# Performance work log

Measured on AMD Instinct MI355X. Metric: run time of the kernel, lower is better.

## Reference

```python
import jax, jax.numpy as jnp
import numpy as np

MIN_NORM = 1e-15
EPS = 4e-3  # fp32 boundary epsilon used by HGCN PoincareBall


def _norm(x):
    return jnp.maximum(jnp.linalg.norm(x, axis=-1, keepdims=True), MIN_NORM)


def _artanh(x):
    return jnp.arctanh(jnp.clip(x, -1.0 + 1e-7, 1.0 - 1e-7))


def proj(x, c):
    # clip points to the open Poincare ball of curvature c
    norm = _norm(x)
    maxnorm = (1.0 - EPS) / jnp.sqrt(c)
    return jnp.where(norm > maxnorm, x / norm * maxnorm, x)


def expmap0(u, c):
    sc = jnp.sqrt(c)
    un = _norm(u)
    return jnp.tanh(sc * un) * u / (sc * un)


def logmap0(p, c):
    sc = jnp.sqrt(c)
    pn = _norm(p)
    return _artanh(sc * pn) * p / (pn * sc)


def mobius_add(x, y, c):
    x2 = jnp.sum(x * x, axis=-1, keepdims=True)
    y2 = jnp.sum(y * y, axis=-1, keepdims=True)
    xy = jnp.sum(x * y, axis=-1, keepdims=True)
    num = (1.0 + 2.0 * c * xy + c * y2) * x + (1.0 - c * x2) * y
    den = 1.0 + 2.0 * c * xy + (c ** 2) * x2 * y2
    return num / jnp.maximum(den, MIN_NORM)


def _mobius_from_mx(mx, x, c):
    # shared tail of mobius_matvec: mx is the Euclidean product, x the input points
    sc = jnp.sqrt(c)
    x_norm = _norm(x)            # [..., 1]
    mx_norm = _norm(mx)          # [..., 1]
    res = jnp.tanh(mx_norm / x_norm * _artanh(sc * x_norm)) * mx / (mx_norm * sc)
    zero_row = jnp.all(mx == 0, axis=-1, keepdims=True)
    return jnp.where(zero_row, jnp.zeros_like(res), res)


def mobius_matvec(m, x, c):
    # standard form: mx = x @ m^T   (m: [out, in], x: [N, in])
    return _mobius_from_mx(x @ m.T, x, c)


def hyp_linear(x, W, b, c):
    hw = proj(expmap0(W, c), c)             # proj_tan0 is identity on PoincareBall
    res = proj(mobius_matvec(hw, x, c), c)
    hb = proj(expmap0(b[None, :], c), c)
    return proj(mobius_add(res, hb, c), c)


def hyp_agg(h, adj, W, b, c):
    hw = proj(expmap0(W, c), c)
    support = mobius_matvec(hw, h, c)       # [N, O]
    # mobius_matvec(support, adj, c): Euclidean part is adj @ support,
    # hyperbolic rescale uses row norms of adj (the 'x' argument)
    out = _mobius_from_mx(adj @ support, adj, c)
    out = mobius_add(out, b[None, :], c)    # raw Euclidean bias, as in source
    return proj(out, c)


def hyp_act(h, c):
    xt = jax.nn.leaky_relu(logmap0(h, c))   # default slope 0.01 == F.leaky_relu
    return proj(expmap0(xt, c), 1.0 - c)    # NOTE: source projects with 1-c


def setup_inputs() -> dict:
    key = jax.random.key(0)
    kx, ka, kw1, kw2, kb2 = jax.random.split(key, 5)
    N, IN, OUT = 8192, 512, 128
    x = jax.random.normal(kx, (N, IN), dtype=jnp.float32) * 0.1
    adj = jax.random.uniform(ka, (N, N), dtype=jnp.float32) * (1.0 / N)
    c = jnp.full((1,), 0.7, dtype=jnp.float32)
    glorot = np.sqrt(6.0 / (IN + OUT))
    lin_weight = jax.random.uniform(kw1, (OUT, IN), minval=-glorot, maxval=glorot, dtype=jnp.float32)
    lin_bias = jnp.zeros((OUT,), dtype=jnp.float32)
    stdv = 1.0 / np.sqrt(OUT)
    agg_weight = jax.random.uniform(kw2, (OUT, OUT), minval=-stdv, maxval=stdv, dtype=jnp.float32)
    agg_bias = jax.random.uniform(kb2, (OUT,), minval=-stdv, maxval=stdv, dtype=jnp.float32)
    return {"x": x, "adj": adj, "c": c, "lin_weight": lin_weight, "lin_bias": lin_bias,
            "agg_weight": agg_weight, "agg_bias": agg_bias}


def reference(x, adj, c, lin_weight, lin_bias, agg_weight, agg_bias):
    h = hyp_linear(x, lin_weight, lin_bias, c)
    h = hyp_agg(h, adj, agg_weight, agg_bias, c)
    return hyp_act(h, c)
```

## Files before the change

### kernel.cpp

```cpp
#include <hip/hip_runtime.h>
#include <math.h>


#define MINN 1e-15f

typedef __bf16 bf16x8 __attribute__((ext_vector_type(8)));
typedef float  f32x4  __attribute__((ext_vector_type(4)));

__device__ __forceinline__ unsigned short f2bf(float f) {
  unsigned int u = __float_as_uint(f);
  u += 0x7FFFu + ((u >> 16) & 1u);
  return (unsigned short)(u >> 16);
}

__device__ __forceinline__ unsigned pk_trunc(float lo, float hi) {
  return __builtin_amdgcn_perm(__float_as_uint(hi), __float_as_uint(lo),
                               0x07060302u);
}

__device__ __forceinline__ float artanh_clip(float z) {
  const float B = (float)(1.0 - 1e-7);
  z = fminf(fmaxf(z, -B), B);
  return 0.5f * logf((1.0f + z) / (1.0f - z));
}

__device__ __forceinline__ float red16(float v) {
  v += __shfl_xor(v, 1, 16);
  v += __shfl_xor(v, 2, 16);
  v += __shfl_xor(v, 4, 16);
  v += __shfl_xor(v, 8, 16);
  return v;
}
__device__ __forceinline__ int red16_and(int v) {
  v &= __shfl_xor(v, 1, 16);
  v &= __shfl_xor(v, 2, 16);
  v &= __shfl_xor(v, 4, 16);
  v &= __shfl_xor(v, 8, 16);
  return v;
}

__device__ __forceinline__ float block_reduce_128(float v, float* red, int t) {
  #pragma unroll
  for (int m = 1; m < 64; m <<= 1) v += __shfl_xor(v, m, 64);
  if ((t & 63) == 0) red[t >> 6] = v;
  __syncthreads();
  return red[0] + red[1];
}

__device__ __forceinline__ size_t bswz(int k, int n) {
  return ((size_t)(((k >> 5) * 8 + (n >> 4)) * 64 + ((k >> 3) & 3) * 16 +
                   (n & 15))) * 8 + (k & 7);
}

__global__ __launch_bounds__(128) void prep_kernel(
    const float* __restrict__ lw, const float* __restrict__ aw,
    const float* __restrict__ lb, const float* __restrict__ cp,
    unsigned short* __restrict__ B1, unsigned short* __restrict__ B2,
    float* __restrict__ hb)
{
  const float c  = cp[0];
  const float sc = sqrtf(c);
  const float maxn = 0.996f / sc;
  const int b = blockIdx.x, t = threadIdx.x;
  __shared__ float red[2];

  if (b < 128) {
    const int o = b;
    float4 v = ((const float4*)(lw + (size_t)o * 512))[t];
    float ss = block_reduce_128(v.x*v.x + v.y*v.y + v.z*v.z + v.w*v.w, red, t);
    float un = fmaxf(sqrtf(ss), MINN);
    float f  = tanhf(sc * un) / (sc * un);
    float nn = f * un;
    if (nn > maxn) f *= maxn / nn;
    float vals[4] = {v.x, v.y, v.z, v.w};
    #pragma unroll
    for (int i = 0; i < 4; ++i)
      B1[bswz(4 * t + i, o)] = f2bf(f * vals[i]);
  } else if (b < 256) {
    const int n = b - 128;
    float v = aw[(size_t)n * 128 + t];
    float ss = block_reduce_128(v * v, red, t);
    float un = fmaxf(sqrtf(ss), MINN);
    float f  = tanhf(sc * un) / (sc * un);
    float nn = f * un;
    if (nn > maxn) f *= maxn / nn;
    B2[bswz(t, n)] = f2bf(f * v);
  } else {
    float v = lb[t];
    float ss = block_reduce_128(v * v, red, t);
    float un = fmaxf(sqrtf(ss), MINN);
    float f  = tanhf(sc * un) / (sc * un);
    float nn = f * un;
    if (nn > maxn) f *= maxn / nn;
    hb[t] = f * v;
  }
}

__global__ __launch_bounds__(256, 2) void hyp_fused12(
    const float* __restrict__ x, const bf16x8* __restrict__ B1f,
    const bf16x8* __restrict__ B2f, const float* __restrict__ cp,
    const float* __restrict__ hbv, unsigned short* __restrict__ B3)
{
  __shared__ __align__(16) float part[4][16][132];
  __shared__ float asw[4][16];
  __shared__ __align__(16) unsigned short h_lds[16][136];
  const int t = threadIdx.x;
  const int w = t >> 6, lane = t & 63;
  const int quad = lane >> 4, l15 = lane & 15;
  const int row0 = blockIdx.x * 16;
  const float c = cp[0], sc = sqrtf(c), maxn = 0.996f / sc;

  f32x4 acc[8] = {};
  float as4[4] = {};
  const float*  Ap = x + (size_t)(row0 + l15) * 512 + w * 128 + quad * 8;
  const bf16x8* Bp = B1f + (size_t)(w * 4) * 512 + lane;

  #pragma unroll
  for (int s = 0; s < 4; ++s) {
    float4 x0 = *(const float4*)(Ap + s * 32);
    float4 x1 = *(const float4*)(Ap + s * 32 + 4);
    as4[0] = fmaf(x0.x, x0.x, fmaf(x0.y, x0.y, as4[0]));
    as4[1] = fmaf(x0.z, x0.z, fmaf(x0.w, x0.w, as4[1]));
    as4[2] = fmaf(x1.x, x1.x, fmaf(x1.y, x1.y, as4[2]));
    as4[3] = fmaf(x1.z, x1.z, fmaf(x1.w, x1.w, as4[3]));
    union { unsigned short us[8]; bf16x8 v; } pk;
    pk.us[0] = f2bf(x0.x); pk.us[1] = f2bf(x0.y);
    pk.us[2] = f2bf(x0.z); pk.us[3] = f2bf(x0.w);
    pk.us[4] = f2bf(x1.x); pk.us[5] = f2bf(x1.y);
    pk.us[6] = f2bf(x1.z); pk.us[7] = f2bf(x1.w);
    #pragma unroll
    for (int i = 0; i < 8; ++i)
      acc[i] = __builtin_amdgcn_mfma_f32_16x16x32_bf16(
                   pk.v, Bp[(size_t)s * 512 + i * 64], acc[i], 0, 0, 0);
  }
  float asum = (as4[0] + as4[1]) + (as4[2] + as4[3]);
  asum += __shfl_xor(asum, 16, 64);
  asum += __shfl_xor(asum, 32, 64);
  #pragma unroll
  for (int i = 0; i < 8; ++i)
    #pragma unroll
    for (int r = 0; r < 4; ++r)
      part[w][quad * 4 + r][i * 16 + l15] = acc[i][r];
  if (lane < 16) asw[w][l15] = asum;
  __syncthreads();

  const int row = t >> 4, j0 = t & 15;
  float v[8];
  #pragma unroll
  for (int i = 0; i < 8; ++i)
    v[i] = part[0][row][j0 * 8 + i] + part[1][row][j0 * 8 + i]
         + part[2][row][j0 * 8 + i] + part[3][row][j0 * 8 + i];
  const float xss = asw[0][row] + asw[1][row] + asw[2][row] + asw[3][row];

  float mxss_l = 0.f; int zf = 1;
  #pragma unroll
  for (int i = 0; i < 8; ++i) { mxss_l += v[i] * v[i]; zf &= (v[i] == 0.f); }
  const float mxss = red16(mxss_l);
  zf = red16_and(zf);

  const float xn  = fmaxf(sqrtf(xss), MINN);
  const float mxn = fmaxf(sqrtf(mxss), MINN);
  float f1 = 0.f;
  if (!zf) f1 = tanhf(mxn / xn * artanh_clip(sc * xn)) / (mxn * sc);

  float g = f1;
  {
    float rn = f1 * mxn;
    if (rn > maxn) g = f1 * (maxn / rn);
  }
  float yv[8];
  {
    float4 q0 = ((const float4*)hbv)[j0 * 2];
    float4 q1 = ((const float4*)hbv)[j0 * 2 + 1];
    yv[0]=q0.x; yv[1]=q0.y; yv[2]=q0.z; yv[3]=q0.w;
    yv[4]=q1.x; yv[5]=q1.y; yv[6]=q1.z; yv[7]=q1.w;
  }
  float xy_l = 0.f, y2_l = 0.f, o8[8];
  #pragma unroll
  for (int i = 0; i < 8; ++i) {
    o8[i] = g * v[i];
    xy_l += o8[i] * yv[i];
    y2_l += yv[i] * yv[i];
  }
  const float xy = red16(xy_l), y2 = red16(y2_l);
  const float x2 = g * g * mxss;
  const float den = fmaxf(1.0f + 2.0f * c * xy + c * c * x2 * y2, MINN);
  const float ca = (1.0f + 2.0f * c * xy + c * y2) / den;
  const float cb = (1.0f - c * x2) / den;
  float h8[8]; float hss_l = 0.f;
  #pragma unroll
  for (int i = 0; i < 8; ++i) {
    h8[i] = ca * o8[i] + cb * yv[i];
    hss_l += h8[i] * h8[i];
  }
  const float hss = red16(hss_l);
  const float hn  = fmaxf(sqrtf(hss), MINN);
  const float s2  = (hn > maxn) ? maxn / hn : 1.0f;
  const float hn2 = fmaxf(s2 * hn, MINN);

  {
    union { unsigned short us[8]; uint4 q; } hp;
    #pragma unroll
    for (int i = 0; i < 8; ++i) hp.us[i] = f2bf(s2 * h8[i]);
    *(uint4*)&h_lds[row][j0 * 8] = hp.q;
  }
  __syncthreads();

  const bf16x8 av2 = *(const bf16x8*)&h_lds[l15][w * 32 + quad * 8];
  f32x4 acc2[8] = {};
  #pragma unroll
  for (int i = 0; i < 8; ++i)
    acc2[i] = __builtin_amdgcn_mfma_f32_16x16x32_bf16(
                  av2, B2f[(size_t)(w * 8 + i) * 64 + lane], acc2[i], 0, 0, 0);
  #pragma unroll
  for (int i = 0; i < 8; ++i)
    #pragma unroll
    for (int r = 0; r < 4; ++r)
      part[w][quad * 4 + r][i * 16 + l15] = acc2[i][r];
  __syncthreads();

  float v2[8];
  #pragma unroll
  for (int i = 0; i < 8; ++i)
    v2[i] = part[0][row][j0 * 8 + i] + part[1][row][j0 * 8 + i]
          + part[2][row][j0 * 8 + i] + part[3][row][j0 * 8 + i];
  float m2l = 0.f; int zf2 = 1;
  #pragma unroll
  for (int i = 0; i < 8; ++i) { m2l += v2[i] * v2[i]; zf2 &= (v2[i] == 0.f); }
  const float mx2ss = red16(m2l);
  zf2 = red16_and(zf2);
  const float mx2n = fmaxf(sqrtf(mx2ss), MINN);
  float f2 = 0.f;
  if (!zf2) f2 = tanhf(mx2n / hn2 * artanh_clip(sc * hn2)) / (mx2n * sc);

  const int k = row0 + row;
  const size_t base = ((size_t)(((k >> 5) * 8 + (j0 >> 1)) * 64 +
                       ((k >> 3) & 3) * 16 + 8 * (j0 & 1))) * 8 + (k & 7);
  #pragma unroll
  for (int i = 0; i < 8; ++i)
    B3[base + (size_t)i * 8] = f2bf(f2 * v2[i]);
}

__global__ __launch_bounds__(512, 2) void hyp_gemm3(
    const float* __restrict__ A, const bf16x8* __restrict__ Bf,
    const float* __restrict__ cp, const float* __restrict__ yvec,
    float* __restrict__ out)
{
  __shared__ __align__(16) unsigned short a_lds[2][32][264];
  const int t = threadIdx.x;
  const int w = t >> 6, lane = t & 63;
  const int quad = lane >> 4, l15 = lane & 15;
  const int wm = w >> 2, wn = w & 3;
  const int row0 = blockIdx.x * 32;
  const float c = cp[0], sc = sqrtf(c), maxn = 0.996f / sc;

  f32x4 acc[2] = {};
  float as4[4] = {};
  const float* Ap = A + (size_t)(row0 + 4 * w) * 8192 + lane * 4;
  const bf16x8* Bw = Bf + (size_t)(2 * wn) * 64 + lane;

  {
    float4 aR[4];
    #pragma unroll
    for (int j = 0; j < 4; ++j) aR[j] = *(const float4*)(Ap + j * 8192);
    #pragma unroll
    for (int j = 0; j < 4; ++j) {
      as4[j] = fmaf(aR[j].x, aR[j].x, fmaf(aR[j].y, aR[j].y,
               fmaf(aR[j].z, aR[j].z, fmaf(aR[j].w, aR[j].w, as4[j]))));
      *(uint2*)&a_lds[0][4 * w + j][lane * 4] =
          make_uint2(pk_trunc(aR[j].x, aR[j].y), pk_trunc(aR[j].z, aR[j].w));
    }
  }
  __syncthreads();

  for (int win = 0; win < 32; ++win) {
    const int cur = win & 1;
    bf16x8 b[8][2];
    #pragma unroll
    for (int ks = 0; ks < 8; ++ks) {
      b[ks][0] = Bw[(size_t)((win * 8 + ks) * 8 + 0) * 64];
      b[ks][1] = Bw[(size_t)((win * 8 + ks) * 8 + 1) * 64];
    }
    float4 aR[4];
    if (win < 31) {
      #pragma unroll
      for (int j = 0; j < 4; ++j)
        aR[j] = *(const float4*)(Ap + j * 8192 + (size_t)(win + 1) * 256);
    }
    #pragma unroll
    for (int ks = 0; ks < 8; ++ks) {
      bf16x8 af = *(const bf16x8*)
          &a_lds[cur][16 * wm + l15][ks * 32 + quad * 8];
      acc[0] = __builtin_amdgcn_mfma_f32_16x16x32_bf16(af, b[ks][0], acc[0],
                                                       0, 0, 0);
      acc[1] = __builtin_amdgcn_mfma_f32_16x16x32_bf16(af, b[ks][1], acc[1],
                                                       0, 0, 0);
    }
    if (win < 31) {
      #pragma unroll
      for (int j = 0; j < 4; ++j) {
        as4[j] = fmaf(aR[j].x, aR[j].x, fmaf(aR[j].y, aR[j].y,
                 fmaf(aR[j].z, aR[j].z, fmaf(aR[j].w, aR[j].w, as4[j]))));
        *(uint2*)&a_lds[cur ^ 1][4 * w + j][lane * 4] =
            make_uint2(pk_trunc(aR[j].x, aR[j].y), pk_trunc(aR[j].z, aR[j].w));
      }
    }
    __syncthreads();
  }

  float (*part)[132] = (float (*)[132]) & a_lds[0][0][0];
  float* asw = (float*)&a_lds[0][0][0] + 32 * 132;

  #pragma unroll
  for (int i = 0; i < 2; ++i)
    #pragma unroll
    for (int r = 0; r < 4; ++r)
      part[16 * wm + quad * 4 + r][32 * wn + 16 * i + l15] = acc[i][r];
  #pragma unroll
  for (int j = 0; j < 4; ++j) {
    float s = as4[j];
    #pragma unroll
    for (int m = 1; m < 64; m <<= 1) s += __shfl_xor(s, m, 64);
    if (lane == 0) asw[4 * w + j] = s;
  }
  __syncthreads();

  const int row = t >> 4, j0 = t & 15;
  float v[8];
  {
    float4 q0 = *(const float4*)&part[row][j0 * 8];
    float4 q1 = *(const float4*)&part[row][j0 * 8 + 4];
    v[0]=q0.x; v[1]=q0.y; v[2]=q0.z; v[3]=q0.w;
    v[4]=q1.x; v[5]=q1.y; v[6]=q1.z; v[7]=q1.w;
  }
  const float xss = asw[row];

  float mxss_l = 0.f; int zf = 1;
  #pragma unroll
  for (int i = 0; i < 8; ++i) { mxss_l += v[i] * v[i]; zf &= (v[i] == 0.f); }
  const float mxss = red16(mxss_l);
  zf = red16_and(zf);

  const float xn  = fmaxf(sqrtf(xss), MINN);
  const float mxn = fmaxf(sqrtf(mxss), MINN);
  float f1 = 0.f;
  if (!zf) f1 = tanhf(mxn / xn * artanh_clip(sc * xn)) / (mxn * sc);

  float yv[8];
  {
    float4 q0 = ((const float4*)yvec)[j0 * 2];
    float4 q1 = ((const float4*)yvec)[j0 * 2 + 1];
    yv[0]=q0.x; yv[1]=q0.y; yv[2]=q0.z; yv[3]=q0.w;
    yv[4]=q1.x; yv[5]=q1.y; yv[6]=q1.z; yv[7]=q1.w;
  }

  float xy_l = 0.f, y2_l = 0.f, o8[8];
  #pragma unroll
  for (int i = 0; i < 8; ++i) {
    o8[i] = f1 * v[i];
    xy_l += o8[i] * yv[i];
    y2_l += yv[i] * yv[i];
  }
  const float xy = red16(xy_l), y2 = red16(y2_l);
  const float x2 = f1 * f1 * mxss;
  const float den = fmaxf(1.0f + 2.0f * c * xy + c * c * x2 * y2, MINN);
  const float ca = (1.0f + 2.0f * c * xy + c * y2) / den;
  const float cb = (1.0f - c * x2) / den;
  float h8[8]; float hss_l = 0.f;
  #pragma unroll
  for (int i = 0; i < 8; ++i) {
    h8[i] = ca * o8[i] + cb * yv[i];
    hss_l += h8[i] * h8[i];
  }
  const float hss = red16(hss_l);
  const float hn  = fmaxf(sqrtf(hss), MINN);
  const float s2  = (hn > maxn) ? maxn / hn : 1.0f;

  const float pn = fmaxf(s2 * hn, MINN);
  const float lf = artanh_clip(sc * pn) / (pn * sc);
  float xt[8]; float uss_l = 0.f;
  #pragma unroll
  for (int i = 0; i < 8; ++i) {
    float l = lf * (s2 * h8[i]);
    xt[i] = (l >= 0.f) ? l : 0.01f * l;
    uss_l += xt[i] * xt[i];
  }
  const float uss = red16(uss_l);
  const float un  = fmaxf(sqrtf(uss), MINN);
  const float ef  = tanhf(sc * un) / (sc * un);
  const float on  = ef * un;
  const float maxn2 = 0.996f / sqrtf(1.0f - c);
  const float s3 = (on > maxn2) ? maxn2 / on : 1.0f;

  float* orow = out + (size_t)(row0 + row) * 128 + j0 * 8;
  *(float4*)orow =
      make_float4(s3*ef*xt[0], s3*ef*xt[1], s3*ef*xt[2], s3*ef*xt[3]);
  *(float4*)(orow + 4) =
      make_float4(s3*ef*xt[4], s3*ef*xt[5], s3*ef*xt[6], s3*ef*xt[7]);
}

extern "C" void kernel_launch(void* const* d_in, const int* in_sizes, int n_in,
                              void* d_out, int out_size, void* d_ws, size_t ws_size,
                              hipStream_t stream)
{
  const float* x   = (const float*)d_in[0];
  const float* adj = (const float*)d_in[1];
  const float* cp  = (const float*)d_in[2];
  const float* lw  = (const float*)d_in[3];
  const float* lb  = (const float*)d_in[4];
  const float* aw  = (const float*)d_in[5];
  const float* ab  = (const float*)d_in[6];
  float* out = (float*)d_out;

  char* ws = (char*)d_ws;
  unsigned short* B1sw = (unsigned short*)(ws);
  unsigned short* B2sw = (unsigned short*)(ws + 131072);
  unsigned short* B3sw = (unsigned short*)(ws + 163840);
  float*          hb   = (float*)(ws + 2260992);

  prep_kernel<<<257, 128, 0, stream>>>(lw, aw, lb, cp, B1sw, B2sw, hb);
  hyp_fused12<<<512, 256, 0, stream>>>(x, (const bf16x8*)B1sw,
                                       (const bf16x8*)B2sw, cp, hb, B3sw);
  hyp_gemm3<<<256, 512, 0, stream>>>(adj, (const bf16x8*)B3sw, cp, ab, out);
}
```

Measured before the change: 408.3 us.

## Halve gemm3 row tile to 16 rows and double grid for more blocks

The adjacency GEMM kernel now handles 16 rows per block instead of 32. Each of its 8 waves computes one 16-column output tile, and the grid doubles to 512 blocks. Launch bounds ask for 4 blocks per CU, aiming to spread the 8192x8192 fp32 adj stream over more CUs and waves so more memory loads are in flight. In exchange every block reads the whole bf16 B3 matrix, so B traffic doubles, and half the threads sit idle in the epilogue.

Result: no change. 407.1 us (-0.3%).

```diff
diff --git a/kernel.cpp b/kernel.cpp
--- a/kernel.cpp
+++ b/kernel.cpp
@@ -241,33 +241,32 @@
     B3[base + (size_t)i * 8] = f2bf(f2 * v2[i]);
 }
 
-__global__ __launch_bounds__(512, 2) void hyp_gemm3(
+__global__ __launch_bounds__(512, 4) void hyp_gemm3(
     const float* __restrict__ A, const bf16x8* __restrict__ Bf,
     const float* __restrict__ cp, const float* __restrict__ yvec,
     float* __restrict__ out)
 {
-  __shared__ __align__(16) unsigned short a_lds[2][32][264];
+  __shared__ __align__(16) unsigned short a_lds[2][16][264];
   const int t = threadIdx.x;
   const int w = t >> 6, lane = t & 63;
   const int quad = lane >> 4, l15 = lane & 15;
-  const int wm = w >> 2, wn = w & 3;
-  const int row0 = blockIdx.x * 32;
+  const int row0 = blockIdx.x * 16;
   const float c = cp[0], sc = sqrtf(c), maxn = 0.996f / sc;
 
-  f32x4 acc[2] = {};
-  float as4[4] = {};
-  const float* Ap = A + (size_t)(row0 + 4 * w) * 8192 + lane * 4;
-  const bf16x8* Bw = Bf + (size_t)(2 * wn) * 64 + lane;
-
-  {
-    float4 aR[4];
-    #pragma unroll
-    for (int j = 0; j < 4; ++j) aR[j] = *(const float4*)(Ap + j * 8192);
-    #pragma unroll
-    for (int j = 0; j < 4; ++j) {
-      as4[j] = fmaf(aR[j].x, aR[j].x, fmaf(aR[j].y, aR[j].y,
-               fmaf(aR[j].z, aR[j].z, fmaf(aR[j].w, aR[j].w, as4[j]))));
-      *(uint2*)&a_lds[0][4 * w + j][lane * 4] =
+  f32x4 acc = {};
+  float as2[2] = {};
+  const float*  Ap = A + (size_t)(row0 + 2 * w) * 8192 + lane * 4;
+  const bf16x8* Bw = Bf + (size_t)w * 64 + lane;
+
+  {
+    float4 aR[2];
+    #pragma unroll
+    for (int j = 0; j < 2; ++j) aR[j] = *(const float4*)(Ap + j * 8192);
+    #pragma unroll
+    for (int j = 0; j < 2; ++j) {
+      as2[j] = fmaf(aR[j].x, aR[j].x, fmaf(aR[j].y, aR[j].y,
+               fmaf(aR[j].z, aR[j].z, fmaf(aR[j].w, aR[j].w, as2[j]))));
+      *(uint2*)&a_lds[0][2 * w + j][lane * 4] =
           make_uint2(pk_trunc(aR[j].x, aR[j].y), pk_trunc(aR[j].z, aR[j].w));
     }
   }
@@ -275,33 +274,27 @@
 
   for (int win = 0; win < 32; ++win) {
     const int cur = win & 1;
-    bf16x8 b[8][2];
-    #pragma unroll
-    for (int ks = 0; ks < 8; ++ks) {
-      b[ks][0] = Bw[(size_t)((win * 8 + ks) * 8 + 0) * 64];
-      b[ks][1] = Bw[(size_t)((win * 8 + ks) * 8 + 1) * 64];
-    }
-    float4 aR[4];
+    bf16x8 b[8];
+    #pragma unroll
+    for (int ks = 0; ks < 8; ++ks)
+      b[ks] = Bw[(size_t)(win * 8 + ks) * 512];
+    float4 aR[2];
     if (win < 31) {
       #pragma unroll
-      for (int j = 0; j < 4; ++j)
+      for (int j = 0; j < 2; ++j)
         aR[j] = *(const float4*)(Ap + j * 8192 + (size_t)(win + 1) * 256);
     }
     #pragma unroll
     for (int ks = 0; ks < 8; ++ks) {
-      bf16x8 af = *(const bf16x8*)
-          &a_lds[cur][16 * wm + l15][ks * 32 + quad * 8];
-      acc[0] = __builtin_amdgcn_mfma_f32_16x16x32_bf16(af, b[ks][0], acc[0],
-                                                       0, 0, 0);
-      acc[1] = __builtin_amdgcn_mfma_f32_16x16x32_bf16(af, b[ks][1], acc[1],
-                                                       0, 0, 0);
+      bf16x8 af = *(const bf16x8*)&a_lds[cur][l15][ks * 32 + quad * 8];
+      acc = __builtin_amdgcn_mfma_f32_16x16x32_bf16(af, b[ks], acc, 0, 0, 0);
     }
     if (win < 31) {
       #pragma unroll
-      for (int j = 0; j < 4; ++j) {
-        as4[j] = fmaf(aR[j].x, aR[j].x, fmaf(aR[j].y, aR[j].y,
-                 fmaf(aR[j].z, aR[j].z, fmaf(aR[j].w, aR[j].w, as4[j]))));
-        *(uint2*)&a_lds[cur ^ 1][4 * w + j][lane * 4] =
+      for (int j = 0; j < 2; ++j) {
+        as2[j] = fmaf(aR[j].x, aR[j].x, fmaf(aR[j].y, aR[j].y,
+                 fmaf(aR[j].z, aR[j].z, fmaf(aR[j].w, aR[j].w, as2[j]))));
+        *(uint2*)&a_lds[cur ^ 1][2 * w + j][lane * 4] =
             make_uint2(pk_trunc(aR[j].x, aR[j].y), pk_trunc(aR[j].z, aR[j].w));
       }
     }
@@ -309,22 +302,21 @@
   }
 
   float (*part)[132] = (float (*)[132]) & a_lds[0][0][0];
-  float* asw = (float*)&a_lds[0][0][0] + 32 * 132;
-
-  #pragma unroll
-  for (int i = 0; i < 2; ++i)
-    #pragma unroll
-    for (int r = 0; r < 4; ++r)
-      part[16 * wm + quad * 4 + r][32 * wn + 16 * i + l15] = acc[i][r];
-  #pragma unroll
-  for (int j = 0; j < 4; ++j) {
-    float s = as4[j];
+  float* asw = (float*)&a_lds[0][0][0] + 16 * 132;
+
+  #pragma unroll
+  for (int r = 0; r < 4; ++r)
+    part[quad * 4 + r][16 * w + l15] = acc[r];
+  #pragma unroll
+  for (int j = 0; j < 2; ++j) {
+    float s = as2[j];
     #pragma unroll
     for (int m = 1; m < 64; m <<= 1) s += __shfl_xor(s, m, 64);
-    if (lane == 0) asw[4 * w + j] = s;
-  }
-  __syncthreads();
-
+    if (lane == 0) asw[2 * w + j] = s;
+  }
+  __syncthreads();
+
+  if (t >= 256) return;
   const int row = t >> 4, j0 = t & 15;
   float v[8];
   {
@@ -421,5 +413,5 @@
   prep_kernel<<<257, 128, 0, stream>>>(lw, aw, lb, cp, B1sw, B2sw, hb);
   hyp_fused12<<<512, 256, 0, stream>>>(x, (const bf16x8*)B1sw,
                                        (const bf16x8*)B2sw, cp, hb, B3sw);
-  hyp_gemm3<<<256, 512, 0, stream>>>(adj, (const bf16x8*)B3sw, cp, ab, out);
-}
+  hyp_gemm3<<<512, 512, 0, stream>>>(adj, (const bf16x8*)B3sw, cp, ab, out);
+}
```
